# Kernel tuning notes

Measured on AMD Instinct MI355X. Metric: run time of the kernel, lower is better.

Reference implementation:

```python
import jax, jax.numpy as jnp
import numpy as np
import math

B, H, S, D = 2, 8, 1024, 384
LAMBDA_INIT = 0.8 - 0.6 * math.exp(-0.3 * 1)  # depth = 1


def _clin(xr, xi, wr, wi, br=None, bi=None):
    # complex linear: (xr + i xi) @ (wr + i wi)^T + (br + i bi)
    o_r = jnp.einsum('bhse,de->bhsd', xr, wr) - jnp.einsum('bhse,de->bhsd', xi, wi)
    o_i = jnp.einsum('bhse,de->bhsd', xr, wi) + jnp.einsum('bhse,de->bhsd', xi, wr)
    if br is not None:
        o_r = o_r + br
        o_i = o_i + bi
    return o_r, o_i


def _attn_w(qr, qi, kr, ki, scale):
    # complex score magnitude -> softmax
    s_r = jnp.einsum('bhqd,bhkd->bhqk', qr, kr) + jnp.einsum('bhqd,bhkd->bhqk', qi, ki)
    s_i = jnp.einsum('bhqd,bhkd->bhqk', qi, kr) - jnp.einsum('bhqd,bhkd->bhqk', qr, ki)
    return jax.nn.softmax(jnp.sqrt(s_r ** 2 + s_i ** 2 + 1e-8) * scale, axis=-1)


def setup_inputs() -> dict:
    key = jax.random.key(0)
    ks = jax.random.split(key, 32)
    n = lambda k, sh, std=1.0: jax.random.normal(k, sh, dtype=jnp.float32) * std
    sd = 1.0 / math.sqrt(D)
    inp = {
        'q_r': n(ks[0], (B, H, S, D)), 'q_i': n(ks[1], (B, H, S, D)),
        'k_r': n(ks[2], (B, H, S, D)), 'k_i': n(ks[3], (B, H, S, D)),
        'v_r': n(ks[4], (B, H, S, D)), 'v_i': n(ks[5], (B, H, S, D)),
        'pe_q_r': n(ks[6], (B, H, S, D)), 'pe_q_i': n(ks[7], (B, H, S, D)),
        'pe_k_r': n(ks[8], (B, H, S, D)), 'pe_k_i': n(ks[9], (B, H, S, D)),
        'wq_r': n(ks[10], (2 * D, D), sd), 'wq_i': n(ks[11], (2 * D, D), sd),
        'bq_r': jnp.zeros((2 * D,), jnp.float32), 'bq_i': jnp.zeros((2 * D,), jnp.float32),
        'wk_r': n(ks[12], (D, D), sd), 'wk_i': n(ks[13], (D, D), sd),
        'bk_r': jnp.zeros((D,), jnp.float32), 'bk_i': jnp.zeros((D,), jnp.float32),
        'wv_r': n(ks[14], (D, D), sd), 'wv_i': n(ks[15], (D, D), sd),
        'bv_r': jnp.zeros((D,), jnp.float32), 'bv_i': jnp.zeros((D,), jnp.float32),
        'wg_r': n(ks[16], (D, D), sd), 'wg_i': n(ks[17], (D, D), sd),
        'bg_r': jnp.zeros((D,), jnp.float32), 'bg_i': jnp.zeros((D,), jnp.float32),
        'wo_r': n(ks[18], (D, D), sd), 'wo_i': n(ks[19], (D, D), sd),
        'bo_r': jnp.zeros((D,), jnp.float32), 'bo_i': jnp.zeros((D,), jnp.float32),
        'lam_q1': n(ks[20], (D,), 0.1), 'lam_k1': n(ks[21], (D,), 0.1),
        'lam_q2': n(ks[22], (D,), 0.1), 'lam_k2': n(ks[23], (D,), 0.1),
        'subln_w': jnp.ones((2 * D,), jnp.float32),
    }
    return inp


def reference(q_r, q_i, k_r, k_i, v_r, v_i, pe_q_r, pe_q_i, pe_k_r, pe_k_i,
              wq_r, wq_i, bq_r, bq_i, wk_r, wk_i, bk_r, bk_i,
              wv_r, wv_i, bv_r, bv_i, wg_r, wg_i, bg_r, bg_i,
              wo_r, wo_i, bo_r, bo_i, lam_q1, lam_k1, lam_q2, lam_k2, subln_w):
    scale = D ** (-0.5)
    qp_r, qp_i = _clin(q_r, q_i, wq_r, wq_i, bq_r, bq_i)   # [B,H,S,2D]
    kp_r, kp_i = _clin(k_r, k_i, wk_r, wk_i, bk_r, bk_i)   # [B,H,S,D]
    vp_r, vp_i = _clin(v_r, v_i, wv_r, wv_i, bv_r, bv_i)
    qp_r = qp_r + jnp.concatenate([pe_q_r, pe_q_r], axis=-1)
    qp_i = qp_i + jnp.concatenate([pe_q_i, pe_q_i], axis=-1)
    kp_r = kp_r + pe_k_r
    kp_i = kp_i + pe_k_i
    q1_r, q2_r = jnp.split(qp_r, 2, axis=-1)
    q1_i, q2_i = jnp.split(qp_i, 2, axis=-1)
    w1 = _attn_w(q1_r, q1_i, kp_r, kp_i, scale)
    w2 = _attn_w(q2_r, q2_i, kp_r, kp_i, scale)
    a1_r = jnp.einsum('bhqk,bhkd->bhqd', w1, vp_r)
    a1_i = jnp.einsum('bhqk,bhkd->bhqd', w1, vp_i)
    a2_r = jnp.einsum('bhqk,bhkd->bhqd', w2, vp_r)
    a2_i = jnp.einsum('bhqk,bhkd->bhqd', w2, vp_i)
    cat_r = jnp.concatenate([a1_r, a2_r], axis=-1)
    cat_i = jnp.concatenate([a1_i, a2_i], axis=-1)
    # complex RMSNorm (SubLN) over 2D dim
    rms = jnp.sqrt(jnp.mean(cat_r ** 2 + cat_i ** 2, axis=-1, keepdims=True) + 1e-5)
    cat_r = cat_r / rms * subln_w
    cat_i = cat_i / rms * subln_w
    a1_r, a2_r = jnp.split(cat_r, 2, axis=-1)
    a1_i, a2_i = jnp.split(cat_i, 2, axis=-1)
    lam1 = jnp.exp(jnp.sum(lam_q1 * lam_k1))
    lam2 = jnp.exp(jnp.sum(lam_q2 * lam_k2))
    lam = jax.nn.sigmoid(lam1 - lam2 + LAMBDA_INIT)
    out_r = a1_r - lam * a2_r
    out_i = a1_i - lam * a2_i
    g_r, g_i = _clin(q_r, q_i, wg_r, wg_i, bg_r, bg_i)
    out_r, out_i = g_r * out_r - g_i * out_i, g_r * out_i + g_i * out_r
    out_r, out_i = _clin(out_r, out_i, wo_r, wo_i, bo_r, bo_i)
    return (out_r, out_i)
```

## Files before the change

kernel.cpp:

```cpp
#include <hip/hip_runtime.h>
#include <cstdint>


typedef _Float16 f16;
typedef __attribute__((ext_vector_type(8))) _Float16 f16x8;
typedef __attribute__((ext_vector_type(4))) _Float16 f16x4;
typedef __attribute__((ext_vector_type(4))) float    f32x4;

#define NROW      16384L
#define HALF_OUT  6291456L
#define SCALE_QK  0.05103103630798288f
#define LAMBDA_INIT 0.35550906759096926f

__device__ __forceinline__ void gl2lds16(const void* g, void* l) {
  __builtin_amdgcn_global_load_lds(
      (const __attribute__((address_space(1))) void*)(uintptr_t)g,
      (__attribute__((address_space(3))) void*)(uint32_t)(uintptr_t)l,
      16, 0, 0);
}

struct PeTab { const float* p[6]; float sgn[6]; };

enum { MODE_PROJ = 0, MODE_VT = 1, MODE_OUT = 2 };

template <int MODE>
__launch_bounds__(256, 2)
__global__ void gemm_kernel(const f16* __restrict__ A, int lda,
                            const f16* __restrict__ W, int ldw,
                            const float* __restrict__ bias, PeTab pe,
                            void* __restrict__ outp, int ldo, int K, int gx)
{
  __shared__ f16 As[2][128 * 32];
  __shared__ f16 Bs[2][128 * 32];
  const int t    = threadIdx.x;
  const int lane = t & 63;
  const int wave = t >> 6;
  const int bid  = blockIdx.x;
  const int xcd  = bid & 7;
  const int per  = bid >> 3;
  const long row0 = (long)(xcd * 16 + per / gx) * 128;
  const long col0 = (long)(per % gx) * 128;
  const f16* Ab = A + row0 * (long)lda;
  const f16* Wb = W + col0 * (long)ldw;

  const int wm = (wave >> 1) * 64;
  const int wn = (wave & 1) * 64;
  const int lm = lane & 15;
  const int lk = (lane >> 4) * 8;

  f32x4 acc[4][4] = {};

  auto stage = [&](int kk, int sub) {
#pragma unroll
    for (int j = 0; j < 2; ++j) {
      int sg = j * 256 + t, r = sg >> 2, c = (sg & 3) << 3;
      gl2lds16(Ab + (long)r * lda + kk + c, &As[sub][sg * 8]);
      gl2lds16(Wb + (long)r * ldw + kk + c, &Bs[sub][sg * 8]);
    }
  };

  stage(0, 0);
  __syncthreads();
  int cur = 0;
  for (int kk = 0; kk < K; kk += 32) {
    if (kk + 32 < K) stage(kk + 32, cur ^ 1);
    f16x8 bfr[4];
#pragma unroll
    for (int nt = 0; nt < 4; ++nt)
      bfr[nt] = *(const f16x8*)&Bs[cur][(wn + nt * 16 + lm) * 32 + lk];
#pragma unroll
    for (int mt = 0; mt < 4; ++mt) {
      f16x8 afr = *(const f16x8*)&As[cur][(wm + mt * 16 + lm) * 32 + lk];
#pragma unroll
      for (int nt = 0; nt < 4; ++nt)
        acc[mt][nt] = __builtin_amdgcn_mfma_f32_16x16x32_f16(afr, bfr[nt], acc[mt][nt], 0, 0, 0);
    }
    __syncthreads();
    cur ^= 1;
  }

  const int lm4 = (lane >> 4) * 4;
  const int ln  = lane & 15;
#pragma unroll
  for (int mt = 0; mt < 4; ++mt) {
#pragma unroll
    for (int nt = 0; nt < 4; ++nt) {
      int col = (int)col0 + wn + nt * 16 + ln;
      if (MODE == MODE_VT) {
        long rowb = row0 + wm + mt * 16 + lm4;
        long bh = rowb >> 10, sx = rowb & 1023;
        f16x4 v;
#pragma unroll
        for (int r = 0; r < 4; ++r) v[r] = (f16)(acc[mt][nt][r] + bias[col]);
        *(f16x4*)&((f16*)outp)[(bh * 768 + col) * 1024 + sx] = v;
      } else {
#pragma unroll
        for (int r = 0; r < 4; ++r) {
          long row = row0 + wm + mt * 16 + lm4 + r;
          float c = acc[mt][nt][r] + bias[col];
          if (MODE == MODE_PROJ) {
            int s2 = col / 384;
            int d  = col - s2 * 384;
            const float* pp = pe.p[s2];
            if (pp) c += pe.sgn[s2] * pp[row * 384 + d];
            ((f16*)outp)[row * (long)ldo + col] = (f16)c;
          } else {
            float* of = (float*)outp;
            if (col < 384) of[row * 384 + col] = c;
            else           of[HALF_OUT + row * 384 + (col - 384)] = c;
          }
        }
      }
    }
  }
}

__launch_bounds__(256, 2)
__global__ void score_kernel(const f16* __restrict__ QG, const f16* __restrict__ Kc,
                             f16* __restrict__ P)
{
  __shared__ f16 AsL[2][128 * 32], AsH[2][128 * 32];
  __shared__ f16 BsL[2][128 * 32], BsH[2][128 * 32];
  const int t = threadIdx.x, lane = t & 63, wave = t >> 6;
  const int bid = blockIdx.x;
  const int xcd = bid & 7, per = bid >> 3;
  const int z   = xcd * 4 + per / 64;
  const int rem = per % 64;
  const int w = z >> 4, bh = z & 15;
  const long row0 = (long)(rem / 8) * 128, col0 = (long)(rem % 8) * 128;
  const f16* A = QG + (long)bh * 1024 * 2304 + row0 * 2304 + w * 768;
  const f16* B = Kc + (long)bh * 1024 * 768 + col0 * 768;
  f16* Pz = P + (long)z * 1024 * 1024;

  const int wm = (wave >> 1) * 64, wn = (wave & 1) * 64;
  const int lm = lane & 15, lk = (lane >> 4) * 8;
  f32x4 accr[4][4] = {}, acci[4][4] = {};

  auto stage = [&](int kk, int sub) {
#pragma unroll
    for (int j = 0; j < 2; ++j) {
      int sg = j * 256 + t, r = sg >> 2, c = (sg & 3) << 3;
      gl2lds16(A + (long)r * 2304 + kk + c,       &AsL[sub][sg * 8]);
      gl2lds16(A + (long)r * 2304 + 384 + kk + c, &AsH[sub][sg * 8]);
      gl2lds16(B + (long)r * 768 + kk + c,        &BsL[sub][sg * 8]);
      gl2lds16(B + (long)r * 768 + 384 + kk + c,  &BsH[sub][sg * 8]);
    }
  };

  stage(0, 0);
  __syncthreads();
  int cur = 0;
  for (int kk = 0; kk < 384; kk += 32) {
    if (kk + 32 < 384) stage(kk + 32, cur ^ 1);
    f16x8 bl[4], bh2[4];
#pragma unroll
    for (int nt = 0; nt < 4; ++nt) {
      bl[nt]  = *(const f16x8*)&BsL[cur][(wn + nt * 16 + lm) * 32 + lk];
      bh2[nt] = *(const f16x8*)&BsH[cur][(wn + nt * 16 + lm) * 32 + lk];
    }
#pragma unroll
    for (int mt = 0; mt < 4; ++mt) {
      f16x8 al  = *(const f16x8*)&AsL[cur][(wm + mt * 16 + lm) * 32 + lk];
      f16x8 ah  = *(const f16x8*)&AsH[cur][(wm + mt * 16 + lm) * 32 + lk];
      f16x8 nal = -al;
#pragma unroll
      for (int nt = 0; nt < 4; ++nt) {
        accr[mt][nt] = __builtin_amdgcn_mfma_f32_16x16x32_f16(al,  bl[nt],  accr[mt][nt], 0, 0, 0);
        accr[mt][nt] = __builtin_amdgcn_mfma_f32_16x16x32_f16(ah,  bh2[nt], accr[mt][nt], 0, 0, 0);
        acci[mt][nt] = __builtin_amdgcn_mfma_f32_16x16x32_f16(ah,  bl[nt],  acci[mt][nt], 0, 0, 0);
        acci[mt][nt] = __builtin_amdgcn_mfma_f32_16x16x32_f16(nal, bh2[nt], acci[mt][nt], 0, 0, 0);
      }
    }
    __syncthreads();
    cur ^= 1;
  }
  const int lm4 = (lane >> 4) * 4, ln = lane & 15;
#pragma unroll
  for (int mt = 0; mt < 4; ++mt)
#pragma unroll
    for (int nt = 0; nt < 4; ++nt) {
      int col = (int)col0 + wn + nt * 16 + ln;
#pragma unroll
      for (int r = 0; r < 4; ++r) {
        long row = row0 + wm + mt * 16 + lm4 + r;
        float sr = accr[mt][nt][r], si = acci[mt][nt][r];
        float m = sqrtf(sr * sr + si * si + 1e-8f) * SCALE_QK;
        Pz[row * 1024 + col] = (f16)m;
      }
    }
}

__launch_bounds__(256, 2)
__global__ void pv_kernel(const f16* __restrict__ P, const f16* __restrict__ Vt,
                          f16* __restrict__ O1, f16* __restrict__ O2)
{
  __shared__ f16 As1[2][128 * 32], As2[2][128 * 32], Bs[2][128 * 32];
  const int t = threadIdx.x, lane = t & 63, wave = t >> 6;
  const int bid = blockIdx.x;
  const int xcd = bid & 7, per = bid >> 3;
  const int bh  = xcd * 2 + per / 48;
  const int rem = per % 48;
  const long row0 = (long)(rem / 6) * 128, col0 = (long)(rem % 6) * 128;
  const f16* A1 = P + ((long)bh << 20) + row0 * 1024;
  const f16* A2 = P + ((long)(16 + bh) << 20) + row0 * 1024;
  const f16* B  = Vt + (long)bh * 768 * 1024 + col0 * 1024;

  const int wm = (wave >> 1) * 64, wn = (wave & 1) * 64;
  const int lm = lane & 15, lk = (lane >> 4) * 8;
  f32x4 ac1[4][4] = {}, ac2[4][4] = {};

  auto stage = [&](int kk, int sub) {
#pragma unroll
    for (int j = 0; j < 2; ++j) {
      int sg = j * 256 + t, r = sg >> 2, c = (sg & 3) << 3;
      gl2lds16(A1 + (long)r * 1024 + kk + c, &As1[sub][sg * 8]);
      gl2lds16(A2 + (long)r * 1024 + kk + c, &As2[sub][sg * 8]);
      gl2lds16(B  + (long)r * 1024 + kk + c, &Bs[sub][sg * 8]);
    }
  };

  stage(0, 0);
  __syncthreads();
  int cur = 0;
  for (int kk = 0; kk < 1024; kk += 32) {
    if (kk + 32 < 1024) stage(kk + 32, cur ^ 1);
    f16x8 bfr[4];
#pragma unroll
    for (int nt = 0; nt < 4; ++nt)
      bfr[nt] = *(const f16x8*)&Bs[cur][(wn + nt * 16 + lm) * 32 + lk];
#pragma unroll
    for (int mt = 0; mt < 4; ++mt) {
      f16x8 a1 = *(const f16x8*)&As1[cur][(wm + mt * 16 + lm) * 32 + lk];
      f16x8 a2 = *(const f16x8*)&As2[cur][(wm + mt * 16 + lm) * 32 + lk];
#pragma unroll
      for (int nt = 0; nt < 4; ++nt) {
        ac1[mt][nt] = __builtin_amdgcn_mfma_f32_16x16x32_f16(a1, bfr[nt], ac1[mt][nt], 0, 0, 0);
        ac2[mt][nt] = __builtin_amdgcn_mfma_f32_16x16x32_f16(a2, bfr[nt], ac2[mt][nt], 0, 0, 0);
      }
    }
    __syncthreads();
    cur ^= 1;
  }
  const int lm4 = (lane >> 4) * 4, ln = lane & 15;
#pragma unroll
  for (int mt = 0; mt < 4; ++mt)
#pragma unroll
    for (int nt = 0; nt < 4; ++nt) {
      int col = (int)col0 + wn + nt * 16 + ln;
#pragma unroll
      for (int r = 0; r < 4; ++r) {
        long row = (long)bh * 1024 + row0 + wm + mt * 16 + lm4 + r;
        O1[row * 768 + col] = (f16)ac1[mt][nt][r];
        O2[row * 768 + col] = (f16)ac2[mt][nt][r];
      }
    }
}

__global__ void softmax_kernel(f16* __restrict__ P)
{
  const long row = (long)blockIdx.x * 4 + (threadIdx.x >> 6);
  f16* p = P + row * 1024;
  const int lane = threadIdx.x & 63;
  f16x8 v0 = *(const f16x8*)(p + lane * 16);
  f16x8 v1 = *(const f16x8*)(p + lane * 16 + 8);
  float x[16];
#pragma unroll
  for (int i = 0; i < 8; ++i) { x[i] = (float)v0[i]; x[8 + i] = (float)v1[i]; }
  float m = x[0];
#pragma unroll
  for (int i = 1; i < 16; ++i) m = fmaxf(m, x[i]);
#pragma unroll
  for (int off = 1; off < 64; off <<= 1) m = fmaxf(m, __shfl_xor(m, off));
  float s = 0.f;
#pragma unroll
  for (int i = 0; i < 16; ++i) { x[i] = __expf(x[i] - m); s += x[i]; }
#pragma unroll
  for (int off = 1; off < 64; off <<= 1) s += __shfl_xor(s, off);
  float inv = 1.f / s;
  f16x8 o0, o1;
#pragma unroll
  for (int i = 0; i < 8; ++i) { o0[i] = (f16)(x[i] * inv); o1[i] = (f16)(x[8 + i] * inv); }
  *(f16x8*)(p + lane * 16)     = o0;
  *(f16x8*)(p + lane * 16 + 8) = o1;
}

__global__ void fuse_kernel(const f16* __restrict__ A1, const f16* __restrict__ A2,
                            const f16* __restrict__ QG, const float* __restrict__ subw,
                            const float* __restrict__ lamp, f16* __restrict__ Xatt)
{
  const long row = blockIdx.x;
  const int t = threadIdx.x, lane = t & 63, wv = t >> 6;
  const f16* a1 = A1 + row * 768;
  const f16* a2 = A2 + row * 768;
  const f16* g  = QG + row * 2304 + 1536;
  float a1r[3], a1i[3], a2r[3], a2i[3];
  float ss = 0.f;
#pragma unroll
  for (int q = 0; q < 3; ++q) {
    int d = t + q * 128;
    a1r[q] = (float)a1[d]; a1i[q] = (float)a1[d + 384];
    a2r[q] = (float)a2[d]; a2i[q] = (float)a2[d + 384];
    ss += a1r[q] * a1r[q] + a1i[q] * a1i[q] + a2r[q] * a2r[q] + a2i[q] * a2i[q];
  }
#pragma unroll
  for (int m = 1; m < 64; m <<= 1) ss += __shfl_xor(ss, m);
  __shared__ float part[2];
  if (lane == 0) part[wv] = ss;
  __syncthreads();
  float inv = rsqrtf((part[0] + part[1]) * (1.f / 768.f) + 1e-5f);
  float lam = lamp[0];
#pragma unroll
  for (int q = 0; q < 3; ++q) {
    int d = t + q * 128;
    float w1 = subw[d], w2 = subw[d + 384];
    float n1r = a1r[q] * inv * w1, n1i = a1i[q] * inv * w1;
    float n2r = a2r[q] * inv * w2, n2i = a2i[q] * inv * w2;
    float orr = n1r - lam * n2r, oii = n1i - lam * n2i;
    float gr = (float)g[d], gi = (float)g[d + 384];
    Xatt[row * 768 + d]       = (f16)(gr * orr - gi * oii);
    Xatt[row * 768 + d + 384] = (f16)(gr * oii + gi * orr);
  }
}

__global__ void lam_kernel(const float* lq1, const float* lk1,
                           const float* lq2, const float* lk2, float* out)
{
  const int t = threadIdx.x, lane = t & 63, wv = t >> 6;
  float s1 = 0.f, s2 = 0.f;
#pragma unroll
  for (int q = 0; q < 3; ++q) {
    int d = t + q * 128;
    s1 += lq1[d] * lk1[d];
    s2 += lq2[d] * lk2[d];
  }
#pragma unroll
  for (int m = 1; m < 64; m <<= 1) { s1 += __shfl_xor(s1, m); s2 += __shfl_xor(s2, m); }
  __shared__ float p1[2], p2[2];
  if (lane == 0) { p1[wv] = s1; p2[wv] = s2; }
  __syncthreads();
  if (t == 0) {
    float x = expf(p1[0] + p1[1]) - expf(p2[0] + p2[1]) + LAMBDA_INIT;
    out[0] = 1.f / (1.f + expf(-x));
  }
}

__global__ void pack_x(const float* __restrict__ xr, const float* __restrict__ xi,
                       f16* __restrict__ X)
{
  long i = (long)blockIdx.x * 256 + threadIdx.x;
  long row = i / 96;
  int  rem = (int)(i - row * 96);
  int  c   = rem * 8;
  const float* src = (c < 384) ? (xr + row * 384 + c) : (xi + row * 384 + (c - 384));
  f16x8 o;
#pragma unroll
  for (int j = 0; j < 8; ++j) o[j] = (f16)src[j];
  *(f16x8*)&X[row * 768 + c] = o;
}

__global__ void pack_wq(const float* wq_r, const float* wq_i,
                        const float* wg_r, const float* wg_i,
                        const float* bq_r, const float* bq_i,
                        const float* bg_r, const float* bg_i,
                        f16* __restrict__ Wp, float* __restrict__ bp)
{
  long i = (long)blockIdx.x * 256 + threadIdx.x;
  int n = (int)(i / 768), e = (int)(i % 768);
  int s = n / 384, d = n - s * 384;
  int hb = (e >= 384);
  int ee = e - hb * 384;
  float v = 0.f, b = 0.f;
  switch (s) {
    case 0: v = hb ? -wq_i[d * 384 + ee]         :  wq_r[d * 384 + ee];         b = bq_r[d];       break;
    case 1: v = hb ?  wq_r[d * 384 + ee]         :  wq_i[d * 384 + ee];         b = bq_i[d];       break;
    case 2: v = hb ? -wq_i[(384 + d) * 384 + ee] :  wq_r[(384 + d) * 384 + ee]; b = bq_r[384 + d]; break;
    case 3: v = hb ?  wq_r[(384 + d) * 384 + ee] :  wq_i[(384 + d) * 384 + ee]; b = bq_i[384 + d]; break;
    case 4: v = hb ? -wg_i[d * 384 + ee]         :  wg_r[d * 384 + ee];         b = bg_r[d];       break;
    case 5: v = hb ?  wg_r[d * 384 + ee]         :  wg_i[d * 384 + ee];         b = bg_i[d];       break;
  }
  Wp[i] = (f16)v;
  if (e == 0) bp[n] = b;
}

__global__ void pack_w_std(const float* wr, const float* wi,
                           const float* br, const float* bi,
                           f16* __restrict__ Wp, float* __restrict__ bp)
{
  long i = (long)blockIdx.x * 256 + threadIdx.x;
  int n = (int)(i / 768), e = (int)(i % 768);
  int hb = (e >= 384);
  int ee = e - hb * 384;
  float v, b;
  if (n < 384) { v = hb ? -wi[n * 384 + ee] : wr[n * 384 + ee]; b = br[n]; }
  else { int d = n - 384; v = hb ? wr[d * 384 + ee] : wi[d * 384 + ee]; b = bi[d]; }
  Wp[i] = (f16)v;
  if (e == 0) bp[n] = b;
}

extern "C" void kernel_launch(void* const* d_in, const int* in_sizes, int n_in,
                              void* d_out, int out_size, void* d_ws, size_t ws_size,
                              hipStream_t stream)
{
  const float* q_r    = (const float*)d_in[0];
  const float* q_i    = (const float*)d_in[1];
  const float* k_r    = (const float*)d_in[2];
  const float* k_i    = (const float*)d_in[3];
  const float* v_r    = (const float*)d_in[4];
  const float* v_i    = (const float*)d_in[5];
  const float* pe_q_r = (const float*)d_in[6];
  const float* pe_q_i = (const float*)d_in[7];
  const float* pe_k_r = (const float*)d_in[8];
  const float* pe_k_i = (const float*)d_in[9];
  const float* wq_r = (const float*)d_in[10];
  const float* wq_i = (const float*)d_in[11];
  const float* bq_r = (const float*)d_in[12];
  const float* bq_i = (const float*)d_in[13];
  const float* wk_r = (const float*)d_in[14];
  const float* wk_i = (const float*)d_in[15];
  const float* bk_r = (const float*)d_in[16];
  const float* bk_i = (const float*)d_in[17];
  const float* wv_r = (const float*)d_in[18];
  const float* wv_i = (const float*)d_in[19];
  const float* bv_r = (const float*)d_in[20];
  const float* bv_i = (const float*)d_in[21];
  const float* wg_r = (const float*)d_in[22];
  const float* wg_i = (const float*)d_in[23];
  const float* bg_r = (const float*)d_in[24];
  const float* bg_i = (const float*)d_in[25];
  const float* wo_r = (const float*)d_in[26];
  const float* wo_i = (const float*)d_in[27];
  const float* bo_r = (const float*)d_in[28];
  const float* bo_i = (const float*)d_in[29];
  const float* lam_q1 = (const float*)d_in[30];
  const float* lam_k1 = (const float*)d_in[31];
  const float* lam_q2 = (const float*)d_in[32];
  const float* lam_k2 = (const float*)d_in[33];
  const float* subln_w = (const float*)d_in[34];

  char* base = (char*)d_ws;
  size_t off = 0;
  auto alloc = [&](size_t bytes) -> void* {
    void* p = base + off;
    off = (off + bytes + 255) & ~(size_t)255;
    return p;
  };
  f16*   Wq   = (f16*)alloc(2304L * 768 * 2);
  f16*   Wk   = (f16*)alloc(768L * 768 * 2);
  f16*   Wv   = (f16*)alloc(768L * 768 * 2);
  f16*   Wo   = (f16*)alloc(768L * 768 * 2);
  float* bq   = (float*)alloc(2304 * 4);
  float* bk   = (float*)alloc(768 * 4);
  float* bv   = (float*)alloc(768 * 4);
  float* bo   = (float*)alloc(768 * 4);
  float* lamp = (float*)alloc(4);
  f16*   X    = (f16*)alloc(NROW * 768 * 2);
  f16*   QG   = (f16*)alloc(NROW * 2304 * 2);
  f16*   Kc   = (f16*)alloc(NROW * 768 * 2);
  f16*   Vt   = (f16*)alloc(16L * 768 * 1024 * 2);
  f16*   P    = (f16*)alloc(32L * 1024 * 1024 * 2);
  if (off > ws_size) return;
  f16* A1   = Kc;
  f16* A2   = X;
  f16* Xatt = Vt;

  pack_wq<<<6912, 256, 0, stream>>>(wq_r, wq_i, wg_r, wg_i, bq_r, bq_i, bg_r, bg_i, Wq, bq);
  pack_w_std<<<2304, 256, 0, stream>>>(wk_r, wk_i, bk_r, bk_i, Wk, bk);
  pack_w_std<<<2304, 256, 0, stream>>>(wv_r, wv_i, bv_r, bv_i, Wv, bv);
  pack_w_std<<<2304, 256, 0, stream>>>(wo_r, wo_i, bo_r, bo_i, Wo, bo);
  lam_kernel<<<1, 128, 0, stream>>>(lam_q1, lam_k1, lam_q2, lam_k2, lamp);

  PeTab pe0{};

  pack_x<<<6144, 256, 0, stream>>>(q_r, q_i, X);
  PeTab peQ{};
  peQ.p[0] = pe_q_r; peQ.sgn[0] = 1.f;
  peQ.p[1] = pe_q_i; peQ.sgn[1] = 1.f;
  peQ.p[2] = pe_q_r; peQ.sgn[2] = 1.f;
  peQ.p[3] = pe_q_i; peQ.sgn[3] = 1.f;
  gemm_kernel<MODE_PROJ><<<2304, 256, 0, stream>>>(
      X, 768, Wq, 768, bq, peQ, QG, 2304, 768, 18);

  pack_x<<<6144, 256, 0, stream>>>(k_r, k_i, X);
  PeTab peK{};
  peK.p[0] = pe_k_r; peK.sgn[0] = 1.f;
  peK.p[1] = pe_k_i; peK.sgn[1] = 1.f;
  gemm_kernel<MODE_PROJ><<<768, 256, 0, stream>>>(
      X, 768, Wk, 768, bk, peK, Kc, 768, 768, 6);

  pack_x<<<6144, 256, 0, stream>>>(v_r, v_i, X);
  gemm_kernel<MODE_VT><<<768, 256, 0, stream>>>(
      X, 768, Wv, 768, bv, pe0, Vt, 0, 768, 6);

  score_kernel<<<2048, 256, 0, stream>>>(QG, Kc, P);
  softmax_kernel<<<8192, 256, 0, stream>>>(P);
  pv_kernel<<<768, 256, 0, stream>>>(P, Vt, A1, A2);

  fuse_kernel<<<16384, 128, 0, stream>>>(A1, A2, QG, subln_w, lamp, Xatt);

  gemm_kernel<MODE_OUT><<<768, 256, 0, stream>>>(
      Xatt, 768, Wo, 768, bo, pe0, d_out, 0, 768, 6);

  (void)in_sizes; (void)n_in; (void)out_size;
}
```

Measured before the change: 787.3 us.

## Triple-buffer LDS staging with vmcnt waits in GEMM, score and PV kernels

Replaces the double-buffered global-to-LDS pipeline with a three-stage ring buffer in the projection GEMM, score and PV kernels. Loads run two tiles ahead, and the kernels wait with explicit s_waitcnt vmcnt counts plus a single barrier per iteration, instead of a full __syncthreads after compute. This is meant to hide more global load latency and cut one barrier per K step. The cost is more LDS per block: the score kernel's launch bound drops to one block per CU, and the other kernels may lose occupancy.

```diff
diff --git a/kernel.cpp b/kernel.cpp
--- a/kernel.cpp
+++ b/kernel.cpp
@@ -30,8 +30,8 @@
                             const float* __restrict__ bias, PeTab pe,
                             void* __restrict__ outp, int ldo, int K, int gx)
 {
-  __shared__ f16 As[2][128 * 32];
-  __shared__ f16 Bs[2][128 * 32];
+  __shared__ f16 As[3][128 * 32];
+  __shared__ f16 Bs[3][128 * 32];
   const int t    = threadIdx.x;
   const int lane = t & 63;
   const int wave = t >> 6;
@@ -59,11 +59,15 @@
     }
   };
 
+  const int NT = K >> 5;
   stage(0, 0);
-  __syncthreads();
+  stage(32, 1);
   int cur = 0;
-  for (int kk = 0; kk < K; kk += 32) {
-    if (kk + 32 < K) stage(kk + 32, cur ^ 1);
+  for (int it = 0; it < NT; ++it) {
+    if (it + 1 < NT) asm volatile("s_waitcnt vmcnt(4)" ::: "memory");
+    else             asm volatile("s_waitcnt vmcnt(0)" ::: "memory");
+    __builtin_amdgcn_s_barrier();
+    if (it + 2 < NT) stage((it + 2) << 5, cur == 0 ? 2 : cur - 1);
     f16x8 bfr[4];
 #pragma unroll
     for (int nt = 0; nt < 4; ++nt)
@@ -75,8 +79,7 @@
       for (int nt = 0; nt < 4; ++nt)
         acc[mt][nt] = __builtin_amdgcn_mfma_f32_16x16x32_f16(afr, bfr[nt], acc[mt][nt], 0, 0, 0);
     }
-    __syncthreads();
-    cur ^= 1;
+    cur = cur == 2 ? 0 : cur + 1;
   }
 
   const int lm4 = (lane >> 4) * 4;
@@ -115,12 +118,12 @@
   }
 }
 
-__launch_bounds__(256, 2)
+__launch_bounds__(256, 1)
 __global__ void score_kernel(const f16* __restrict__ QG, const f16* __restrict__ Kc,
                              f16* __restrict__ P)
 {
-  __shared__ f16 AsL[2][128 * 32], AsH[2][128 * 32];
-  __shared__ f16 BsL[2][128 * 32], BsH[2][128 * 32];
+  __shared__ f16 AsL[3][128 * 32], AsH[3][128 * 32];
+  __shared__ f16 BsL[3][128 * 32], BsH[3][128 * 32];
   const int t = threadIdx.x, lane = t & 63, wave = t >> 6;
   const int bid = blockIdx.x;
   const int xcd = bid & 7, per = bid >> 3;
@@ -147,11 +150,15 @@
     }
   };
 
+  const int NT = 12;
   stage(0, 0);
-  __syncthreads();
+  stage(32, 1);
   int cur = 0;
-  for (int kk = 0; kk < 384; kk += 32) {
-    if (kk + 32 < 384) stage(kk + 32, cur ^ 1);
+  for (int it = 0; it < NT; ++it) {
+    if (it + 1 < NT) asm volatile("s_waitcnt vmcnt(8)" ::: "memory");
+    else             asm volatile("s_waitcnt vmcnt(0)" ::: "memory");
+    __builtin_amdgcn_s_barrier();
+    if (it + 2 < NT) stage((it + 2) << 5, cur == 0 ? 2 : cur - 1);
     f16x8 bl[4], bh2[4];
 #pragma unroll
     for (int nt = 0; nt < 4; ++nt) {
@@ -171,8 +178,7 @@
         acci[mt][nt] = __builtin_amdgcn_mfma_f32_16x16x32_f16(nal, bh2[nt], acci[mt][nt], 0, 0, 0);
       }
     }
-    __syncthreads();
-    cur ^= 1;
+    cur = cur == 2 ? 0 : cur + 1;
   }
   const int lm4 = (lane >> 4) * 4, ln = lane & 15;
 #pragma unroll
@@ -194,7 +200,7 @@
 __global__ void pv_kernel(const f16* __restrict__ P, const f16* __restrict__ Vt,
                           f16* __restrict__ O1, f16* __restrict__ O2)
 {
-  __shared__ f16 As1[2][128 * 32], As2[2][128 * 32], Bs[2][128 * 32];
+  __shared__ f16 As1[3][128 * 32], As2[3][128 * 32], Bs[3][128 * 32];
   const int t = threadIdx.x, lane = t & 63, wave = t >> 6;
   const int bid = blockIdx.x;
   const int xcd = bid & 7, per = bid >> 3;
@@ -219,11 +225,15 @@
     }
   };
 
+  const int NT = 32;
   stage(0, 0);
-  __syncthreads();
+  stage(32, 1);
   int cur = 0;
-  for (int kk = 0; kk < 1024; kk += 32) {
-    if (kk + 32 < 1024) stage(kk + 32, cur ^ 1);
+  for (int it = 0; it < NT; ++it) {
+    if (it + 1 < NT) asm volatile("s_waitcnt vmcnt(6)" ::: "memory");
+    else             asm volatile("s_waitcnt vmcnt(0)" ::: "memory");
+    __builtin_amdgcn_s_barrier();
+    if (it + 2 < NT) stage((it + 2) << 5, cur == 0 ? 2 : cur - 1);
     f16x8 bfr[4];
 #pragma unroll
     for (int nt = 0; nt < 4; ++nt)
@@ -238,8 +248,7 @@
         ac2[mt][nt] = __builtin_amdgcn_mfma_f32_16x16x32_f16(a2, bfr[nt], ac2[mt][nt], 0, 0, 0);
       }
     }
-    __syncthreads();
-    cur ^= 1;
+    cur = cur == 2 ? 0 : cur + 1;
   }
   const int lm4 = (lane >> 4) * 4, ln = lane & 15;
 #pragma unroll
```

Measured after the change: 822.2 us. 4.4% more time.

## Move GEMMs to 256x256 tiles with 512 threads and swizzled LDS

Applied to the files above, without the earlier changes.

Replaces the 128x128, K=32 GEMM and score kernels with 256-wide tiles, 512-thread blocks, K=64 stages and an XOR-swizzled LDS layout that avoids bank conflicts. The score kernel now reads the Q slab as one contiguous K=768 pass and pairs it with K and half-swapped K, negating the operand in the first half. The separate PV kernel is folded into the generic GEMM, with the two attention branches stacked as extra rows. The aim is more data reuse per LDS load and fewer bank conflicts. In exchange each block uses much more LDS, which limits occupancy, and several launches (192 blocks) no longer fill every CU.

```diff
diff --git a/kernel.cpp b/kernel.cpp
--- a/kernel.cpp
+++ b/kernel.cpp
@@ -21,78 +21,111 @@
 
 struct PeTab { const float* p[6]; float sgn[6]; };
 
-enum { MODE_PROJ = 0, MODE_VT = 1, MODE_OUT = 2 };
+enum { MODE_PROJ = 0, MODE_VT = 1, MODE_OUT = 2, MODE_PV = 3 };
 
 template <int MODE>
-__launch_bounds__(256, 2)
-__global__ void gemm_kernel(const f16* __restrict__ A, int lda,
-                            const f16* __restrict__ W, int ldw,
-                            const float* __restrict__ bias, PeTab pe,
-                            void* __restrict__ outp, int ldo, int K, int gx)
-{
-  __shared__ f16 As[2][128 * 32];
-  __shared__ f16 Bs[2][128 * 32];
+__launch_bounds__(512, 2)
+__global__ void gemm256(const f16* __restrict__ A, int lda,
+                        const f16* __restrict__ W, int ldw,
+                        const float* __restrict__ bias, PeTab pe,
+                        void* __restrict__ outp, void* __restrict__ outp2,
+                        int ldo, int K, int gx)
+{
+  __shared__ f16 As[2][256 * 64];
+  __shared__ f16 Bs[2][256 * 64];
   const int t    = threadIdx.x;
   const int lane = t & 63;
   const int wave = t >> 6;
   const int bid  = blockIdx.x;
   const int xcd  = bid & 7;
   const int per  = bid >> 3;
-  const long row0 = (long)(xcd * 16 + per / gx) * 128;
-  const long col0 = (long)(per % gx) * 128;
-  const f16* Ab = A + row0 * (long)lda;
-  const f16* Wb = W + col0 * (long)ldw;
-
-  const int wm = (wave >> 1) * 64;
-  const int wn = (wave & 1) * 64;
+
+  long row0, col0;
+  const f16 *Ab, *Wb;
+  int bh = 0;
+  if (MODE == MODE_PV) {
+    const int pd3 = per / 3;
+    const int ntile = per - pd3 * 3;
+    const int mt_g = xcd * 16 + pd3;
+    bh   = mt_g >> 3;
+    row0 = (long)(mt_g & 7) * 256;
+    col0 = (long)ntile * 256;
+    Ab = A + ((long)(bh + (row0 >= 1024 ? 16 : 0)) << 20) + (row0 & 1023) * (long)lda;
+    Wb = W + (long)bh * 768 * 1024 + col0 * (long)ldw;
+  } else {
+    row0 = (long)(xcd * 8 + per / gx) * 256;
+    col0 = (long)(per % gx) * 256;
+    Ab = A + row0 * (long)lda;
+    Wb = W + col0 * (long)ldw;
+  }
+
+  const int wm = (wave >> 2) * 128;
+  const int wn = (wave & 3) * 64;
   const int lm = lane & 15;
-  const int lk = (lane >> 4) * 8;
-
-  f32x4 acc[4][4] = {};
+  const int l4 = lane >> 4;
+
+  f32x4 acc[8][4] = {};
 
   auto stage = [&](int kk, int sub) {
 #pragma unroll
-    for (int j = 0; j < 2; ++j) {
-      int sg = j * 256 + t, r = sg >> 2, c = (sg & 3) << 3;
-      gl2lds16(Ab + (long)r * lda + kk + c, &As[sub][sg * 8]);
-      gl2lds16(Wb + (long)r * ldw + kk + c, &Bs[sub][sg * 8]);
+    for (int p = 0; p < 4; ++p) {
+      int sg = p * 512 + t;
+      int r = sg >> 3, cl = sg & 7;
+      int cg = cl ^ (r & 7);
+      gl2lds16(Ab + (long)r * lda + kk + cg * 8, &As[sub][sg * 8]);
+      gl2lds16(Wb + (long)r * ldw + kk + cg * 8, &Bs[sub][sg * 8]);
     }
   };
 
+  const int NT = K >> 6;
   stage(0, 0);
-  __syncthreads();
+  asm volatile("s_waitcnt vmcnt(0)\ns_barrier" ::: "memory");
   int cur = 0;
-  for (int kk = 0; kk < K; kk += 32) {
-    if (kk + 32 < K) stage(kk + 32, cur ^ 1);
-    f16x8 bfr[4];
-#pragma unroll
-    for (int nt = 0; nt < 4; ++nt)
-      bfr[nt] = *(const f16x8*)&Bs[cur][(wn + nt * 16 + lm) * 32 + lk];
-#pragma unroll
-    for (int mt = 0; mt < 4; ++mt) {
-      f16x8 afr = *(const f16x8*)&As[cur][(wm + mt * 16 + lm) * 32 + lk];
-#pragma unroll
-      for (int nt = 0; nt < 4; ++nt)
-        acc[mt][nt] = __builtin_amdgcn_mfma_f32_16x16x32_f16(afr, bfr[nt], acc[mt][nt], 0, 0, 0);
-    }
-    __syncthreads();
+  for (int it = 0; it < NT; ++it) {
+    if (it + 1 < NT) stage((it + 1) << 6, cur ^ 1);
+#pragma unroll
+    for (int ks = 0; ks < 2; ++ks) {
+      f16x8 bfr[4];
+#pragma unroll
+      for (int nt = 0; nt < 4; ++nt) {
+        int rr = wn + nt * 16 + lm;
+        bfr[nt] = *(const f16x8*)&Bs[cur][rr * 64 + (((ks * 4 + l4) ^ (rr & 7)) * 8)];
+      }
+#pragma unroll
+      for (int mt = 0; mt < 8; ++mt) {
+        int rr = wm + mt * 16 + lm;
+        f16x8 afr = *(const f16x8*)&As[cur][rr * 64 + (((ks * 4 + l4) ^ (rr & 7)) * 8)];
+#pragma unroll
+        for (int nt = 0; nt < 4; ++nt)
+          acc[mt][nt] = __builtin_amdgcn_mfma_f32_16x16x32_f16(afr, bfr[nt], acc[mt][nt], 0, 0, 0);
+      }
+    }
+    asm volatile("s_waitcnt vmcnt(0)\ns_barrier" ::: "memory");
     cur ^= 1;
   }
 
-  const int lm4 = (lane >> 4) * 4;
-  const int ln  = lane & 15;
-#pragma unroll
-  for (int mt = 0; mt < 4; ++mt) {
+  const int lm4 = l4 * 4;
+  const int ln  = lm;
+#pragma unroll
+  for (int mt = 0; mt < 8; ++mt) {
 #pragma unroll
     for (int nt = 0; nt < 4; ++nt) {
       int col = (int)col0 + wn + nt * 16 + ln;
       if (MODE == MODE_VT) {
         long rowb = row0 + wm + mt * 16 + lm4;
-        long bh = rowb >> 10, sx = rowb & 1023;
+        long vbh = rowb >> 10, sx = rowb & 1023;
         f16x4 v;
 #pragma unroll
         for (int r = 0; r < 4; ++r) v[r] = (f16)(acc[mt][nt][r] + bias[col]);
-        *(f16x4*)&((f16*)outp)[(bh * 768 + col) * 1024 + sx] = v;
+        *(f16x4*)&((f16*)outp)[(vbh * 768 + col) * 1024 + sx] = v;
+      } else if (MODE == MODE_PV) {
+#pragma unroll
+        for (int r = 0; r < 4; ++r) {
+          long grow = row0 + wm + mt * 16 + lm4 + r;
+          f16 val = (f16)acc[mt][nt][r];
+          if (grow < 1024) ((f16*)outp )[((long)bh * 1024 + grow)        * 768 + col] = val;
+          else             ((f16*)outp2)[((long)bh * 1024 + grow - 1024) * 768 + col] = val;
+        }
       } else {
 #pragma unroll
         for (int r = 0; r < 4; ++r) {
@@ -115,66 +148,81 @@
   }
 }
 
-__launch_bounds__(256, 2)
-__global__ void score_kernel(const f16* __restrict__ QG, const f16* __restrict__ Kc,
-                             f16* __restrict__ P)
-{
-  __shared__ f16 AsL[2][128 * 32], AsH[2][128 * 32];
-  __shared__ f16 BsL[2][128 * 32], BsH[2][128 * 32];
+__launch_bounds__(512, 2)
+__global__ void score256(const f16* __restrict__ QG, const f16* __restrict__ Kc,
+                         f16* __restrict__ P)
+{
+  __shared__ f16 As[2][256 * 64];
+  __shared__ f16 Bs[2][128 * 64];
+  __shared__ f16 Cs[2][128 * 64];
   const int t = threadIdx.x, lane = t & 63, wave = t >> 6;
   const int bid = blockIdx.x;
   const int xcd = bid & 7, per = bid >> 3;
-  const int z   = xcd * 4 + per / 64;
-  const int rem = per % 64;
-  const int w = z >> 4, bh = z & 15;
-  const long row0 = (long)(rem / 8) * 128, col0 = (long)(rem % 8) * 128;
-  const f16* A = QG + (long)bh * 1024 * 2304 + row0 * 2304 + w * 768;
-  const f16* B = Kc + (long)bh * 1024 * 768 + col0 * 768;
-  f16* Pz = P + (long)z * 1024 * 1024;
-
-  const int wm = (wave >> 1) * 64, wn = (wave & 1) * 64;
-  const int lm = lane & 15, lk = (lane >> 4) * 8;
+  const int slab = xcd * 4 + (per >> 5);
+  const int tile = per & 31;
+  const int w = slab >> 4, bh = slab & 15;
+  const long row0 = (long)(tile >> 3) * 256;
+  const long col0 = (long)(tile & 7) * 128;
+  const f16* Ab = QG + (long)bh * 1024 * 2304 + row0 * 2304 + w * 768;
+  const f16* Bb = Kc + (long)bh * 1024 * 768 + col0 * 768;
+
+  const int wm = (wave >> 1) * 64;
+  const int wn = (wave & 1) * 64;
+  const int lm = lane & 15, l4 = lane >> 4;
+
   f32x4 accr[4][4] = {}, acci[4][4] = {};
 
   auto stage = [&](int kk, int sub) {
-#pragma unroll
-    for (int j = 0; j < 2; ++j) {
-      int sg = j * 256 + t, r = sg >> 2, c = (sg & 3) << 3;
-      gl2lds16(A + (long)r * 2304 + kk + c,       &AsL[sub][sg * 8]);
-      gl2lds16(A + (long)r * 2304 + 384 + kk + c, &AsH[sub][sg * 8]);
-      gl2lds16(B + (long)r * 768 + kk + c,        &BsL[sub][sg * 8]);
-      gl2lds16(B + (long)r * 768 + 384 + kk + c,  &BsH[sub][sg * 8]);
+    int kk2 = kk < 384 ? kk + 384 : kk - 384;
+#pragma unroll
+    for (int p = 0; p < 4; ++p) {
+      int sg = p * 512 + t;
+      int r = sg >> 3, cl = sg & 7, cg = cl ^ (r & 7);
+      gl2lds16(Ab + (long)r * 2304 + kk + cg * 8, &As[sub][sg * 8]);
+    }
+#pragma unroll
+    for (int p = 0; p < 2; ++p) {
+      int sg = p * 512 + t;
+      int r = sg >> 3, cl = sg & 7, cg = cl ^ (r & 7);
+      gl2lds16(Bb + (long)r * 768 + kk  + cg * 8, &Bs[sub][sg * 8]);
+      gl2lds16(Bb + (long)r * 768 + kk2 + cg * 8, &Cs[sub][sg * 8]);
     }
   };
 
   stage(0, 0);
-  __syncthreads();
+  asm volatile("s_waitcnt vmcnt(0)\ns_barrier" ::: "memory");
   int cur = 0;
-  for (int kk = 0; kk < 384; kk += 32) {
-    if (kk + 32 < 384) stage(kk + 32, cur ^ 1);
-    f16x8 bl[4], bh2[4];
-#pragma unroll
-    for (int nt = 0; nt < 4; ++nt) {
-      bl[nt]  = *(const f16x8*)&BsL[cur][(wn + nt * 16 + lm) * 32 + lk];
-      bh2[nt] = *(const f16x8*)&BsH[cur][(wn + nt * 16 + lm) * 32 + lk];
-    }
-#pragma unroll
-    for (int mt = 0; mt < 4; ++mt) {
-      f16x8 al  = *(const f16x8*)&AsL[cur][(wm + mt * 16 + lm) * 32 + lk];
-      f16x8 ah  = *(const f16x8*)&AsH[cur][(wm + mt * 16 + lm) * 32 + lk];
-      f16x8 nal = -al;
+  for (int it = 0; it < 12; ++it) {
+    if (it + 1 < 12) stage((it + 1) << 6, cur ^ 1);
+    const bool neg = (it < 6);
+#pragma unroll
+    for (int ks = 0; ks < 2; ++ks) {
+      f16x8 bfr[4], cfr[4];
 #pragma unroll
       for (int nt = 0; nt < 4; ++nt) {
-        accr[mt][nt] = __builtin_amdgcn_mfma_f32_16x16x32_f16(al,  bl[nt],  accr[mt][nt], 0, 0, 0);
-        accr[mt][nt] = __builtin_amdgcn_mfma_f32_16x16x32_f16(ah,  bh2[nt], accr[mt][nt], 0, 0, 0);
-        acci[mt][nt] = __builtin_amdgcn_mfma_f32_16x16x32_f16(ah,  bl[nt],  acci[mt][nt], 0, 0, 0);
-        acci[mt][nt] = __builtin_amdgcn_mfma_f32_16x16x32_f16(nal, bh2[nt], acci[mt][nt], 0, 0, 0);
-      }
-    }
-    __syncthreads();
+        int rr = wn + nt * 16 + lm;
+        int off = rr * 64 + (((ks * 4 + l4) ^ (rr & 7)) * 8);
+        bfr[nt] = *(const f16x8*)&Bs[cur][off];
+        cfr[nt] = *(const f16x8*)&Cs[cur][off];
+      }
+#pragma unroll
+      for (int mt = 0; mt < 4; ++mt) {
+        int rr = wm + mt * 16 + lm;
+        f16x8 a  = *(const f16x8*)&As[cur][rr * 64 + (((ks * 4 + l4) ^ (rr & 7)) * 8)];
+        f16x8 am = neg ? -a : a;
+#pragma unroll
+        for (int nt = 0; nt < 4; ++nt) {
+          accr[mt][nt] = __builtin_amdgcn_mfma_f32_16x16x32_f16(a,  bfr[nt], accr[mt][nt], 0, 0, 0);
+          acci[mt][nt] = __builtin_amdgcn_mfma_f32_16x16x32_f16(am, cfr[nt], acci[mt][nt], 0, 0, 0);
+        }
+      }
+    }
+    asm volatile("s_waitcnt vmcnt(0)\ns_barrier" ::: "memory");
     cur ^= 1;
   }
-  const int lm4 = (lane >> 4) * 4, ln = lane & 15;
+
+  f16* Pz = P + ((long)slab << 20);
+  const int lm4 = l4 * 4, ln = lm;
 #pragma unroll
   for (int mt = 0; mt < 4; ++mt)
 #pragma unroll
@@ -186,72 +234,6 @@
         float sr = accr[mt][nt][r], si = acci[mt][nt][r];
         float m = sqrtf(sr * sr + si * si + 1e-8f) * SCALE_QK;
         Pz[row * 1024 + col] = (f16)m;
-      }
-    }
-}
-
-__launch_bounds__(256, 2)
-__global__ void pv_kernel(const f16* __restrict__ P, const f16* __restrict__ Vt,
-                          f16* __restrict__ O1, f16* __restrict__ O2)
-{
-  __shared__ f16 As1[2][128 * 32], As2[2][128 * 32], Bs[2][128 * 32];
-  const int t = threadIdx.x, lane = t & 63, wave = t >> 6;
-  const int bid = blockIdx.x;
-  const int xcd = bid & 7, per = bid >> 3;
-  const int bh  = xcd * 2 + per / 48;
-  const int rem = per % 48;
-  const long row0 = (long)(rem / 6) * 128, col0 = (long)(rem % 6) * 128;
-  const f16* A1 = P + ((long)bh << 20) + row0 * 1024;
-  const f16* A2 = P + ((long)(16 + bh) << 20) + row0 * 1024;
-  const f16* B  = Vt + (long)bh * 768 * 1024 + col0 * 1024;
-
-  const int wm = (wave >> 1) * 64, wn = (wave & 1) * 64;
-  const int lm = lane & 15, lk = (lane >> 4) * 8;
-  f32x4 ac1[4][4] = {}, ac2[4][4] = {};
-
-  auto stage = [&](int kk, int sub) {
-#pragma unroll
-    for (int j = 0; j < 2; ++j) {
-      int sg = j * 256 + t, r = sg >> 2, c = (sg & 3) << 3;
-      gl2lds16(A1 + (long)r * 1024 + kk + c, &As1[sub][sg * 8]);
-      gl2lds16(A2 + (long)r * 1024 + kk + c, &As2[sub][sg * 8]);
-      gl2lds16(B  + (long)r * 1024 + kk + c, &Bs[sub][sg * 8]);
-    }
-  };
-
-  stage(0, 0);
-  __syncthreads();
-  int cur = 0;
-  for (int kk = 0; kk < 1024; kk += 32) {
-    if (kk + 32 < 1024) stage(kk + 32, cur ^ 1);
-    f16x8 bfr[4];
-#pragma unroll
-    for (int nt = 0; nt < 4; ++nt)
-      bfr[nt] = *(const f16x8*)&Bs[cur][(wn + nt * 16 + lm) * 32 + lk];
-#pragma unroll
-    for (int mt = 0; mt < 4; ++mt) {
-      f16x8 a1 = *(const f16x8*)&As1[cur][(wm + mt * 16 + lm) * 32 + lk];
-      f16x8 a2 = *(const f16x8*)&As2[cur][(wm + mt * 16 + lm) * 32 + lk];
-#pragma unroll
-      for (int nt = 0; nt < 4; ++nt) {
-        ac1[mt][nt] = __builtin_amdgcn_mfma_f32_16x16x32_f16(a1, bfr[nt], ac1[mt][nt], 0, 0, 0);
-        ac2[mt][nt] = __builtin_amdgcn_mfma_f32_16x16x32_f16(a2, bfr[nt], ac2[mt][nt], 0, 0, 0);
-      }
-    }
-    __syncthreads();
-    cur ^= 1;
-  }
-  const int lm4 = (lane >> 4) * 4, ln = lane & 15;
-#pragma unroll
-  for (int mt = 0; mt < 4; ++mt)
-#pragma unroll
-    for (int nt = 0; nt < 4; ++nt) {
-      int col = (int)col0 + wn + nt * 16 + ln;
-#pragma unroll
-      for (int r = 0; r < 4; ++r) {
-        long row = (long)bh * 1024 + row0 + wm + mt * 16 + lm4 + r;
-        O1[row * 768 + col] = (f16)ac1[mt][nt][r];
-        O2[row * 768 + col] = (f16)ac2[mt][nt][r];
       }
     }
 }
@@ -477,28 +459,29 @@
   peQ.p[1] = pe_q_i; peQ.sgn[1] = 1.f;
   peQ.p[2] = pe_q_r; peQ.sgn[2] = 1.f;
   peQ.p[3] = pe_q_i; peQ.sgn[3] = 1.f;
-  gemm_kernel<MODE_PROJ><<<2304, 256, 0, stream>>>(
-      X, 768, Wq, 768, bq, peQ, QG, 2304, 768, 18);
+  gemm256<MODE_PROJ><<<576, 512, 0, stream>>>(
+      X, 768, Wq, 768, bq, peQ, QG, nullptr, 2304, 768, 9);
 
   pack_x<<<6144, 256, 0, stream>>>(k_r, k_i, X);
   PeTab peK{};
   peK.p[0] = pe_k_r; peK.sgn[0] = 1.f;
   peK.p[1] = pe_k_i; peK.sgn[1] = 1.f;
-  gemm_kernel<MODE_PROJ><<<768, 256, 0, stream>>>(
-      X, 768, Wk, 768, bk, peK, Kc, 768, 768, 6);
+  gemm256<MODE_PROJ><<<192, 512, 0, stream>>>(
+      X, 768, Wk, 768, bk, peK, Kc, nullptr, 768, 768, 3);
 
   pack_x<<<6144, 256, 0, stream>>>(v_r, v_i, X);
-  gemm_kernel<MODE_VT><<<768, 256, 0, stream>>>(
-      X, 768, Wv, 768, bv, pe0, Vt, 0, 768, 6);
-
-  score_kernel<<<2048, 256, 0, stream>>>(QG, Kc, P);
+  gemm256<MODE_VT><<<192, 512, 0, stream>>>(
+      X, 768, Wv, 768, bv, pe0, Vt, nullptr, 0, 768, 3);
+
+  score256<<<1024, 512, 0, stream>>>(QG, Kc, P);
   softmax_kernel<<<8192, 256, 0, stream>>>(P);
-  pv_kernel<<<768, 256, 0, stream>>>(P, Vt, A1, A2);
+  gemm256<MODE_PV><<<384, 512, 0, stream>>>(
+      P, 1024, Vt, 1024, nullptr, pe0, A1, A2, 0, 1024, 0);
 
   fuse_kernel<<<16384, 128, 0, stream>>>(A1, A2, QG, subln_w, lamp, Xatt);
 
-  gemm_kernel<MODE_OUT><<<768, 256, 0, stream>>>(
-      Xatt, 768, Wo, 768, bo, pe0, d_out, 0, 768, 6);
+  gemm256<MODE_OUT><<<192, 512, 0, stream>>>(
+      Xatt, 768, Wo, 768, bo, pe0, d_out, nullptr, 0, 768, 3);
 
   (void)in_sizes; (void)n_in; (void)out_size;
 }
```

After: 841.6 us. 1.07x slower.
